# Optimization experiments

Hardware: AMD Instinct MI355X
Metric: run time of the kernel (lower is better)

## Reference

```python
import jax, jax.numpy as jnp
import numpy as np

TEMPERATURE = 0.1
EPS = 1e-8  # matches torch F.cosine_similarity eps


def setup_inputs() -> dict:
    key = jax.random.key(0)
    feats = jax.random.normal(key, (8192, 256), dtype=jnp.float32)
    return {"feats": feats}


def reference(feats) -> jnp.ndarray:
    n = feats.shape[0]
    # cosine similarity = normalized feats GEMM (avoids O(N^2 D) intermediate)
    norms = jnp.maximum(jnp.linalg.norm(feats, axis=-1, keepdims=True), EPS)
    fn = feats / norms  # [N, D]
    sim = jnp.einsum('nd,md->nm', fn, fn) / TEMPERATURE  # [N, N]
    eye = jnp.eye(n, dtype=bool)
    masked_sim = jnp.where(eye, -jnp.inf, sim)
    lse = jax.nn.logsumexp(masked_sim, axis=-1)  # [N]
    # torch.roll(masked_sim, n//2, 0).diag()[i] == masked_sim[(i - n//2) % n, i]
    idx = jnp.arange(n)
    pos = masked_sim[(idx - n // 2) % n, idx]  # [N]
    loss = lse - pos
    return jnp.mean(loss)
```

## Files before the change

### kernel.cpp

```cpp
#include <hip/hip_runtime.h>
#include <hip/hip_bf16.h>
#include <math.h>

typedef __attribute__((ext_vector_type(8))) short short8;
typedef __attribute__((ext_vector_type(4))) float f32x4;

#define N 8192
#define D 256
#define INV_T 10.0f
#define EPSN 1e-8f

__device__ __forceinline__ unsigned short f2bf(float x) {
  unsigned int u = __float_as_uint(x);
  u += 0x7fffu + ((u >> 16) & 1u);
  return (unsigned short)(u >> 16);
}

__device__ __forceinline__ void async16(void* lds, const void* g) {
  __builtin_amdgcn_global_load_lds(
      (const __attribute__((address_space(1))) void*)g,
      (__attribute__((address_space(3))) void*)lds,
      16, 0, 0);
}

__device__ __forceinline__ float rowsum16(float v) {
  v += __uint_as_float(__builtin_amdgcn_update_dpp(
      0u, __float_as_uint(v), 0x118, 0xf, 0xf, true));
  v += __uint_as_float(__builtin_amdgcn_update_dpp(
      0u, __float_as_uint(v), 0x114, 0xf, 0xf, true));
  v += __uint_as_float(__builtin_amdgcn_update_dpp(
      0u, __float_as_uint(v), 0x112, 0xf, 0xf, true));
  v += __uint_as_float(__builtin_amdgcn_update_dpp(
      0u, __float_as_uint(v), 0x111, 0xf, 0xf, true));
  return v;
}

__global__ __launch_bounds__(256) void normalize_k(const float* __restrict__ feats,
                                                   unsigned short* __restrict__ fn,
                                                   float* __restrict__ rowsum,
                                                   float* __restrict__ out) {
  int row = blockIdx.x * 4 + (threadIdx.x >> 6);
  int lane = threadIdx.x & 63;
  if (threadIdx.x < 4) rowsum[blockIdx.x * 4 + threadIdx.x] = 0.0f;
  if (blockIdx.x == 0 && threadIdx.x == 0) out[0] = 0.0f;
  float4 v = ((const float4*)(feats + (size_t)row * D))[lane];
  float ss = v.x * v.x + v.y * v.y + v.z * v.z + v.w * v.w;
#pragma unroll
  for (int off = 32; off; off >>= 1) ss += __shfl_xor(ss, off, 64);
  float inv = 1.0f / fmaxf(sqrtf(ss), EPSN);
  uint2 o;
  o.x = (unsigned)f2bf(v.x * inv) | ((unsigned)f2bf(v.y * inv) << 16);
  o.y = (unsigned)f2bf(v.z * inv) | ((unsigned)f2bf(v.w * inv) << 16);
  ((uint2*)(fn + (size_t)row * D))[lane] = o;
}

__global__ __launch_bounds__(512) void gemm_lse(const unsigned short* __restrict__ fn,
                                                float* __restrict__ rowsum,
                                                float* __restrict__ pos) {
  __shared__ unsigned short As[2][128 * 64];
  __shared__ unsigned short Bs[2][128 * 64];
  __shared__ float lrow[128];
  __shared__ float lcol[128];
  int tid = threadIdx.x;
  int wave = tid >> 6, lane = tid & 63;
  int wm = wave >> 2, wn = wave & 3;
  int hi = lane >> 4, lo = lane & 15;

  int b = blockIdx.x;
  int t = (b & 7) * 260 + (b >> 3);
  int bm = (int)((129.0 - sqrt((double)(16641 - 8 * t))) * 0.5);
  int S = bm * (129 - bm) / 2;
  if (t < S) { --bm; S = bm * (129 - bm) / 2; }
  else { int S1 = (bm + 1) * (128 - bm) / 2; if (t >= S1) { ++bm; S = S1; } }
  int bn = bm + (t - S);

  const char* fb = (const char*)fn;

  auto stage = [&](int buf, int kt) {
    int k0b = kt * 128;
#pragma unroll
    for (int inst = 0; inst < 2; ++inst) {
      int o = tid * 16 + inst * 8192;
      int r = o >> 7;
      int cs = (o & 127) ^ ((r & 7) << 4);
      const char* ga = fb + (size_t)(bm * 128 + r) * (D * 2) + k0b + cs;
      const char* gb = fb + (size_t)(bn * 128 + r) * (D * 2) + k0b + cs;
      async16((char*)&As[buf][0] + o, ga);
      async16((char*)&Bs[buf][0] + o, gb);
    }
  };

  f32x4 acc[4][2];
#pragma unroll
  for (int m = 0; m < 4; ++m)
#pragma unroll
    for (int n = 0; n < 2; ++n) acc[m][n] = (f32x4){0.f, 0.f, 0.f, 0.f};

  auto compute = [&](int buf) {
#pragma unroll
    for (int ks = 0; ks < 2; ++ks) {
      int cbyte = ks * 64 + hi * 16;
      short8 af[4], bfr[2];
#pragma unroll
      for (int m = 0; m < 4; ++m) {
        int R = wm * 64 + m * 16 + lo;
        af[m] = *(const short8*)((const char*)&As[buf][0] + R * 128 +
                                 (cbyte ^ ((R & 7) << 4)));
      }
#pragma unroll
      for (int n = 0; n < 2; ++n) {
        int R = wn * 32 + n * 16 + lo;
        bfr[n] = *(const short8*)((const char*)&Bs[buf][0] + R * 128 +
                                  (cbyte ^ ((R & 7) << 4)));
      }
#pragma unroll
      for (int m = 0; m < 4; ++m)
#pragma unroll
        for (int n = 0; n < 2; ++n)
          acc[m][n] = __builtin_amdgcn_mfma_f32_16x16x32_bf16(af[m], bfr[n],
                                                              acc[m][n], 0, 0, 0);
    }
  };

  stage(0, 0);
  stage(1, 1);
  if (tid < 128) { lrow[tid] = 0.0f; lcol[tid] = 0.0f; }

#pragma unroll
  for (int kt = 0; kt < 4; ++kt) {
    if (kt < 3) asm volatile("s_waitcnt vmcnt(4)" ::: "memory");
    else        asm volatile("s_waitcnt vmcnt(0)" ::: "memory");
    __builtin_amdgcn_s_barrier();
    __builtin_amdgcn_sched_barrier(0);
    compute(kt & 1);
    asm volatile("s_waitcnt lgkmcnt(0)" ::: "memory");
    __builtin_amdgcn_sched_barrier(0);
    __builtin_amdgcn_s_barrier();
    if (kt < 2) stage(kt & 1, kt + 2);
  }

  bool isdiag = (bm == bn);
  float ca[2] = {0.f, 0.f};
  int rbase = wm * 64, cbase = wn * 32;
#pragma unroll
  for (int m = 0; m < 4; ++m) {
#pragma unroll
    for (int j = 0; j < 4; ++j) {
      int rloc = rbase + m * 16 + hi * 4 + j;
      float v = 0.f;
#pragma unroll
      for (int n = 0; n < 2; ++n) {
        float e = __expf(fmaf(acc[m][n][j], 10.0f, -10.0f));
        if (isdiag && rloc == cbase + n * 16 + lo) e = 0.f;
        v += e;
        ca[n] += e;
      }
      v = rowsum16(v);
      if (lo == 15) atomicAdd(&lrow[rloc], v);
    }
  }
  if (!isdiag) {
#pragma unroll
    for (int n = 0; n < 2; ++n) {
      float c = ca[n];
      c += __shfl_xor(c, 16, 64);
      c += __shfl_xor(c, 32, 64);
      if (hi == 0) atomicAdd(&lcol[cbase + n * 16 + lo], c);
    }
  }
  if (bn == bm + 32) {
#pragma unroll
    for (int m = 0; m < 4; ++m) {
      int rb = wm * 64 + m * 16;
#pragma unroll
      for (int n = 0; n < 2; ++n) {
        if (rb == wn * 32 + n * 16 && (lo >> 2) == hi) {
          int j = lo & 3;
          f32x4 a = acc[m][n];
          float pv = (j == 0) ? a[0] : (j == 1) ? a[1] : (j == 2) ? a[2] : a[3];
          pv *= INV_T;
          int gr = bm * 128 + rb + lo;
          pos[gr] = pv;
          pos[gr + N / 2] = pv;
        }
      }
    }
  }
  __syncthreads();
  if (tid < 128) {
    atomicAdd(&rowsum[bm * 128 + tid], lrow[tid]);
    if (!isdiag) atomicAdd(&rowsum[bn * 128 + tid], lcol[tid]);
  }
}

__global__ __launch_bounds__(256) void final_k(const float* __restrict__ rowsum,
                                               const float* __restrict__ pos,
                                               float* __restrict__ out) {
  int tid = threadIdx.x;
  int i = blockIdx.x * 256 + tid;
  float s = 10.0f + logf(rowsum[i]) - pos[i];
#pragma unroll
  for (int off = 32; off; off >>= 1) s += __shfl_xor(s, off, 64);
  __shared__ float red[4];
  if ((tid & 63) == 0) red[tid >> 6] = s;
  __syncthreads();
  if (tid == 0)
    atomicAdd(out, (red[0] + red[1] + red[2] + red[3]) * (1.0f / N));
}

extern "C" void kernel_launch(void* const* d_in, const int* in_sizes, int n_in,
                              void* d_out, int out_size, void* d_ws, size_t ws_size,
                              hipStream_t stream) {
  const float* feats = (const float*)d_in[0];
  float* out = (float*)d_out;
  char* ws = (char*)d_ws;
  unsigned short* fn = (unsigned short*)ws;
  float* pos = (float*)(ws + 4 * 1024 * 1024);
  float* rowsum = (float*)(ws + 4 * 1024 * 1024 + 32 * 1024);

  normalize_k<<<N / 4, 256, 0, stream>>>(feats, fn, rowsum, out);
  gemm_lse<<<(64 * 65) / 2, 512, 0, stream>>>(fn, rowsum, pos);
  final_k<<<32, 256, 0, stream>>>(rowsum, pos, out);
}
```

Before: 44.94 us.

## Switch normalized features and similarity GEMM from bf16 to fp8 MFMA

Normalized features are now quantized to fp8 instead of bf16, and the similarity GEMM uses the fp8 16x16x32 MFMA with a new 64-byte-row LDS swizzle and precomputed fragment offsets. Operand bytes and LDS traffic are halved, staging needs one async load per matrix per K tile instead of two, and launch bounds request higher occupancy. In exchange the similarities lose precision, which after scaling by 10 and exponentiating may move the loss beyond tolerance.

```diff
diff --git a/kernel.cpp b/kernel.cpp
--- a/kernel.cpp
+++ b/kernel.cpp
@@ -2,19 +2,12 @@
 #include <hip/hip_bf16.h>
 #include <math.h>
 
-typedef __attribute__((ext_vector_type(8))) short short8;
 typedef __attribute__((ext_vector_type(4))) float f32x4;
 
 #define N 8192
 #define D 256
 #define INV_T 10.0f
 #define EPSN 1e-8f
-
-__device__ __forceinline__ unsigned short f2bf(float x) {
-  unsigned int u = __float_as_uint(x);
-  u += 0x7fffu + ((u >> 16) & 1u);
-  return (unsigned short)(u >> 16);
-}
 
 __device__ __forceinline__ void async16(void* lds, const void* g) {
   __builtin_amdgcn_global_load_lds(
@@ -36,7 +29,7 @@
 }
 
 __global__ __launch_bounds__(256) void normalize_k(const float* __restrict__ feats,
-                                                   unsigned short* __restrict__ fn,
+                                                   unsigned char* __restrict__ fn,
                                                    float* __restrict__ rowsum,
                                                    float* __restrict__ out) {
   int row = blockIdx.x * 4 + (threadIdx.x >> 6);
@@ -48,17 +41,16 @@
 #pragma unroll
   for (int off = 32; off; off >>= 1) ss += __shfl_xor(ss, off, 64);
   float inv = 1.0f / fmaxf(sqrtf(ss), EPSN);
-  uint2 o;
-  o.x = (unsigned)f2bf(v.x * inv) | ((unsigned)f2bf(v.y * inv) << 16);
-  o.y = (unsigned)f2bf(v.z * inv) | ((unsigned)f2bf(v.w * inv) << 16);
-  ((uint2*)(fn + (size_t)row * D))[lane] = o;
-}
-
-__global__ __launch_bounds__(512) void gemm_lse(const unsigned short* __restrict__ fn,
-                                                float* __restrict__ rowsum,
-                                                float* __restrict__ pos) {
-  __shared__ unsigned short As[2][128 * 64];
-  __shared__ unsigned short Bs[2][128 * 64];
+  int w = __builtin_amdgcn_cvt_pk_fp8_f32(v.x * inv, v.y * inv, 0, false);
+  w = __builtin_amdgcn_cvt_pk_fp8_f32(v.z * inv, v.w * inv, w, true);
+  ((int*)(fn + (size_t)row * D))[lane] = w;
+}
+
+__global__ __launch_bounds__(512, 8) void gemm_lse(const unsigned char* __restrict__ fn,
+                                                   float* __restrict__ rowsum,
+                                                   float* __restrict__ pos) {
+  __shared__ unsigned char As[2][8192];
+  __shared__ unsigned char Bs[2][8192];
   __shared__ float lrow[128];
   __shared__ float lcol[128];
   int tid = threadIdx.x;
@@ -74,22 +66,33 @@
   else { int S1 = (bm + 1) * (128 - bm) / 2; if (t >= S1) { ++bm; S = S1; } }
   int bn = bm + (t - S);
 
-  const char* fb = (const char*)fn;
-
+  int sr = tid >> 2;
+  int sc = (tid & 3) ^ ((sr >> 1) & 3);
+  const unsigned char* gsa = fn + (size_t)(bm * 128 + sr) * D + sc * 16;
+  const unsigned char* gsb = fn + (size_t)(bn * 128 + sr) * D + sc * 16;
   auto stage = [&](int buf, int kt) {
-    int k0b = kt * 128;
-#pragma unroll
-    for (int inst = 0; inst < 2; ++inst) {
-      int o = tid * 16 + inst * 8192;
-      int r = o >> 7;
-      int cs = (o & 127) ^ ((r & 7) << 4);
-      const char* ga = fb + (size_t)(bm * 128 + r) * (D * 2) + k0b + cs;
-      const char* gb = fb + (size_t)(bn * 128 + r) * (D * 2) + k0b + cs;
-      async16((char*)&As[buf][0] + o, ga);
-      async16((char*)&Bs[buf][0] + o, gb);
-    }
+    async16(&As[buf][tid * 16], gsa + kt * 64);
+    async16(&Bs[buf][tid * 16], gsb + kt * 64);
   };
 
+  int offA[4][2], offB[2][2];
+#pragma unroll
+  for (int m = 0; m < 4; ++m) {
+    int R = wm * 64 + m * 16 + lo;
+#pragma unroll
+    for (int ks = 0; ks < 2; ++ks)
+      offA[m][ks] = R * 64 + ((((ks << 1) | (hi >> 1)) ^ ((R >> 1) & 3)) << 4) +
+                    ((hi & 1) << 3);
+  }
+#pragma unroll
+  for (int n = 0; n < 2; ++n) {
+    int R = wn * 32 + n * 16 + lo;
+#pragma unroll
+    for (int ks = 0; ks < 2; ++ks)
+      offB[n][ks] = R * 64 + ((((ks << 1) | (hi >> 1)) ^ ((R >> 1) & 3)) << 4) +
+                    ((hi & 1) << 3);
+  }
+
   f32x4 acc[4][2];
 #pragma unroll
   for (int m = 0; m < 4; ++m)
@@ -99,26 +102,19 @@
   auto compute = [&](int buf) {
 #pragma unroll
     for (int ks = 0; ks < 2; ++ks) {
-      int cbyte = ks * 64 + hi * 16;
-      short8 af[4], bfr[2];
-#pragma unroll
-      for (int m = 0; m < 4; ++m) {
-        int R = wm * 64 + m * 16 + lo;
-        af[m] = *(const short8*)((const char*)&As[buf][0] + R * 128 +
-                                 (cbyte ^ ((R & 7) << 4)));
-      }
-#pragma unroll
-      for (int n = 0; n < 2; ++n) {
-        int R = wn * 32 + n * 16 + lo;
-        bfr[n] = *(const short8*)((const char*)&Bs[buf][0] + R * 128 +
-                                  (cbyte ^ ((R & 7) << 4)));
-      }
+      long long a[4], bb[2];
 #pragma unroll
       for (int m = 0; m < 4; ++m)
+        a[m] = *(const long long*)&As[buf][offA[m][ks]];
+#pragma unroll
+      for (int n = 0; n < 2; ++n)
+        bb[n] = *(const long long*)&Bs[buf][offB[n][ks]];
+#pragma unroll
+      for (int m = 0; m < 4; ++m)
 #pragma unroll
         for (int n = 0; n < 2; ++n)
-          acc[m][n] = __builtin_amdgcn_mfma_f32_16x16x32_bf16(af[m], bfr[n],
-                                                              acc[m][n], 0, 0, 0);
+          acc[m][n] = __builtin_amdgcn_mfma_f32_16x16x32_fp8_fp8(
+              a[m], bb[n], acc[m][n], 0, 0, 0);
     }
   };
 
@@ -128,7 +124,7 @@
 
 #pragma unroll
   for (int kt = 0; kt < 4; ++kt) {
-    if (kt < 3) asm volatile("s_waitcnt vmcnt(4)" ::: "memory");
+    if (kt < 3) asm volatile("s_waitcnt vmcnt(2)" ::: "memory");
     else        asm volatile("s_waitcnt vmcnt(0)" ::: "memory");
     __builtin_amdgcn_s_barrier();
     __builtin_amdgcn_sched_barrier(0);
@@ -214,9 +210,9 @@
   const float* feats = (const float*)d_in[0];
   float* out = (float*)d_out;
   char* ws = (char*)d_ws;
-  unsigned short* fn = (unsigned short*)ws;
-  float* pos = (float*)(ws + 4 * 1024 * 1024);
-  float* rowsum = (float*)(ws + 4 * 1024 * 1024 + 32 * 1024);
+  unsigned char* fn = (unsigned char*)ws;
+  float* pos = (float*)(ws + 2 * 1024 * 1024);
+  float* rowsum = (float*)(ws + 2 * 1024 * 1024 + 32 * 1024);
 
   normalize_k<<<N / 4, 256, 0, stream>>>(feats, fn, rowsum, out);
   gemm_lse<<<(64 * 65) / 2, 512, 0, stream>>>(fn, rowsum, pos);
```

Measured after the change: 39.00 us. -13.2%, faster.
